# Kernel optimization log

Measured on AMD Instinct MI355X. Metric: run time of the kernel, lower is better.

The kernel has to match this reference:

```python
import jax, jax.numpy as jnp
import numpy as np

C1, C2, K, S, P, D = 128, 128, 3, 1, 1, 1
B, H, W = 16, 64, 64
K2 = K * K


def conv2d(x, w, b=None, stride=1, pad=1, dil=1):
    y = jax.lax.conv_general_dilated(
        x, w, (stride, stride), [(pad, pad), (pad, pad)],
        rhs_dilation=(dil, dil), dimension_numbers=('NCHW', 'OIHW', 'NCHW'))
    if b is not None:
        y = y + b[None, :, None, None]
    return y


def setup_inputs() -> dict:
    key = jax.random.key(0)
    ks = jax.random.split(key, 6)
    fan = C1 * K * K
    x = jax.random.normal(ks[0], (B, C1, H, W), jnp.float32)
    w_conv = jax.random.normal(ks[1], (C2, C1, K, K), jnp.float32) / np.sqrt(fan)
    # small offset / mask branch weights -> realistic small learned offsets
    w_off = jax.random.normal(ks[2], (2 * K2, C1, K, K), jnp.float32) * 0.01
    b_off = jnp.zeros((2 * K2,), jnp.float32)
    w_mask = jax.random.normal(ks[3], (K2, C1, K, K), jnp.float32) * 0.01
    b_mask = jnp.zeros((K2,), jnp.float32)
    return {'x': x, 'w_conv': w_conv, 'w_off': w_off, 'b_off': b_off,
            'w_mask': w_mask, 'b_mask': b_mask}


def _deform_conv(x, offset, mask, w_conv):
    Bv, _, Hv, Wv = x.shape
    Ho, Wo = offset.shape[2], offset.shape[3]
    off = offset.reshape(Bv, K2, 2, Ho, Wo)
    off_y, off_x = off[:, :, 0], off[:, :, 1]
    # base sampling grid: out pixel + kernel tap (stride/pad/dilation)
    hs = (jnp.arange(Ho) * S - P).astype(jnp.float32)
    ws = (jnp.arange(Wo) * S - P).astype(jnp.float32)
    n = jnp.arange(K2)
    ky = ((n // K) * D).astype(jnp.float32)
    kx = ((n % K) * D).astype(jnp.float32)
    py = off_y + hs[None, None, :, None] + ky[None, :, None, None]  # [B,K2,Ho,Wo]
    px = off_x + ws[None, None, None, :] + kx[None, :, None, None]

    y0 = jnp.floor(py)
    x0 = jnp.floor(px)
    wy1 = py - y0
    wx1 = px - x0
    wy0 = 1.0 - wy1
    wx0 = 1.0 - wx1
    y0i = y0.astype(jnp.int32)
    x0i = x0.astype(jnp.int32)

    gather = jax.vmap(lambda xb, yi, xi: xb[:, yi, xi])  # -> [B,C,K2,Ho,Wo]

    def corner(yc, xc, wgt):
        valid = (yc >= 0) & (yc < Hv) & (xc >= 0) & (xc < Wv)
        yi = jnp.clip(yc, 0, Hv - 1)
        xi = jnp.clip(xc, 0, Wv - 1)
        v = gather(x, yi, xi)
        return v * (wgt * valid)[:, None]

    samp = (corner(y0i, x0i, wy0 * wx0)
            + corner(y0i, x0i + 1, wy0 * wx1)
            + corner(y0i + 1, x0i, wy1 * wx0)
            + corner(y0i + 1, x0i + 1, wy1 * wx1))  # [B,C1,K2,Ho,Wo]
    samp = samp * mask[:, None]
    wk = w_conv.reshape(C2, C1, K2)
    return jnp.einsum('bcnhw,ocn->bohw', samp, wk)


def reference(x, w_conv, w_off, b_off, w_mask, b_mask):
    offset = conv2d(x, w_off, b_off, S, P, D)
    mask = jax.nn.sigmoid(conv2d(x, w_mask, b_mask, S, P, D))
    return _deform_conv(x, offset, mask, w_conv)
```

## Files before the change

### kernel.cpp

```cpp
#include <hip/hip_runtime.h>
#include <math.h>

#define B_   16
#define C1_  128
#define C2_  128
#define H_   64
#define W_   64
#define HW_  4096
#define NCH_ 27

typedef __attribute__((ext_vector_type(8))) short  bf16x8;
typedef __attribute__((ext_vector_type(8))) unsigned short u16x8;
typedef __attribute__((ext_vector_type(4))) float  f32x4;
typedef __attribute__((ext_vector_type(4))) unsigned int u32x4;

__device__ __forceinline__ unsigned short f2bf(float f) {
  unsigned int u = __builtin_bit_cast(unsigned int, f);
  u += 0x7fff + ((u >> 16) & 1);
  return (unsigned short)(u >> 16);
}
__device__ __forceinline__ float lo16(unsigned int u) {
  return __builtin_bit_cast(float, u << 16);
}
__device__ __forceinline__ float hi16(unsigned int u) {
  return __builtin_bit_cast(float, u & 0xffff0000u);
}

__global__ __launch_bounds__(256) void prep_k(
    const float* __restrict__ x, unsigned short* __restrict__ xcl,
    const float* __restrict__ wc, unsigned short* __restrict__ wpk,
    const float* __restrict__ w_off, const float* __restrict__ w_mask,
    unsigned short* __restrict__ wob) {
  __shared__ unsigned short tile[128][66];
  int blk = blockIdx.x;
  int t = threadIdx.x;

  if (blk < 1024) {
    int bid = blk;
    int bh = ((bid & 7) << 7) | (bid >> 3);
    int b = bh >> 6, h = bh & 63;
    int wv = t & 63, cq = t >> 6;
    const float* xb = x + ((size_t)b * 128) * HW_ + h * 64;
#pragma unroll
    for (int i = 0; i < 32; ++i) {
      int c = i * 4 + cq;
      tile[c][wv] = f2bf(xb[(size_t)c * HW_ + wv]);
    }
    __syncthreads();
    int w2 = t >> 2, cg = (t & 3) * 32;
    unsigned short* op = xcl + (((size_t)bh) * 64 + w2) * 128 + cg;
#pragma unroll
    for (int i = 0; i < 4; ++i) {
      u16x8 pk;
#pragma unroll
      for (int j = 0; j < 8; ++j) pk[j] = tile[cg + i * 8 + j][w2];
      *reinterpret_cast<u16x8*>(op + i * 8) = pk;
    }
  } else if (blk < 1024 + 576) {
    int idx = (blk - 1024) * 256 + t;
    if (idx >= 9 * 8 * 4 * 64 * 8) return;
    int j  = idx & 7;
    int l  = (idx >> 3) & 63;
    int kb = (idx >> 9) & 3;
    int ot = (idx >> 11) & 7;
    int n  = idx >> 14;
    int oc = ot * 16 + (l & 15);
    int c  = kb * 32 + (l >> 4) * 8 + j;
    wpk[idx] = f2bf(wc[(oc * 128 + c) * 9 + n]);
  } else {
    int idx = (blk - 1024 - 576) * 256 + t;
    if (idx >= 2 * 36 * 64 * 8) return;
    int j = idx & 7;
    int l = (idx >> 3) & 63;
    int rest = idx >> 9;
    int s = rest % 36;
    int nt = rest / 36;
    int ch = nt * 16 + (l & 15);
    int n = s >> 2;
    int c = (s & 3) * 32 + (l >> 4) * 8 + j;
    float v = 0.f;
    if (ch < 18) v = w_off[((ch * 128) + c) * 9 + n];
    else if (ch < 27) v = w_mask[(((ch - 18) * 128) + c) * 9 + n];
    wob[idx] = f2bf(v);
  }
}

__global__ __launch_bounds__(256) void offmask_k(
    const unsigned short* __restrict__ xcl,
    const unsigned short* __restrict__ wob,
    const float* __restrict__ b_off, const float* __restrict__ b_mask,
    float* __restrict__ om) {
  __shared__ __attribute__((aligned(16))) char xr[3 * 66 * 256];
  int bid = blockIdx.x;
  int bh = ((bid & 7) << 7) | (bid >> 3);
  int b = bh >> 6, h = bh & 63;
  int t = threadIdx.x;
  int l = t & 63, w = t >> 6;

#pragma unroll
  for (int ky = 0; ky < 3; ++ky) {
    int hh = h - 1 + ky;
    bool valid = (unsigned)hh < 64u;
    const unsigned short* src = xcl + (((size_t)b * 64 + (valid ? hh : 0)) * 64) * 128;
#pragma unroll
    for (int i = 0; i < 4; ++i) {
      int m = t + i * 256;
      int px = m >> 4;
      int c2 = (m & 15) * 16;
      unsigned off = (unsigned)((ky * 66 + px + 1) * 256 + c2) ^ (((px + 1) & 7) << 4);
      u16x8 v = {0, 0, 0, 0, 0, 0, 0, 0};
      if (valid) v = *reinterpret_cast<const u16x8*>(src + (size_t)m * 8);
      *reinterpret_cast<u16x8*>(xr + off) = v;
    }
  }
  if (t < 96) {
    int r = t >> 5, rem = t & 31;
    int slot = (rem < 16) ? 0 : 65;
    int c2 = (rem & 15) * 16;
    unsigned off = (unsigned)((r * 66 + slot) * 256 + c2) ^ ((slot & 7) << 4);
    u16x8 z = {0, 0, 0, 0, 0, 0, 0, 0};
    *reinterpret_cast<u16x8*>(xr + off) = z;
  }
  __syncthreads();

  f32x4 acc0 = (f32x4)0.f, acc1 = (f32x4)0.f;
#pragma unroll
  for (int n = 0; n < 9; ++n) {
    int ky = n / 3, kx = n % 3;
    int slot = w * 16 + (l & 15) + kx;
#pragma unroll
    for (int cs = 0; cs < 4; ++cs) {
      int s = n * 4 + cs;
      unsigned aoff = (unsigned)((ky * 66 + slot) * 256 + (l >> 4) * 16 + cs * 64)
                      ^ ((unsigned)(slot & 7) << 4);
      bf16x8 afr = *reinterpret_cast<const bf16x8*>(xr + aoff);
      bf16x8 bf0 = *reinterpret_cast<const bf16x8*>(wob + ((size_t)(0 * 36 + s) * 64 + l) * 8);
      bf16x8 bf1 = *reinterpret_cast<const bf16x8*>(wob + ((size_t)(1 * 36 + s) * 64 + l) * 8);
      acc0 = __builtin_amdgcn_mfma_f32_16x16x32_bf16(afr, bf0, acc0, 0, 0, 0);
      acc1 = __builtin_amdgcn_mfma_f32_16x16x32_bf16(afr, bf1, acc1, 0, 0, 0);
    }
  }

  int pxo = w * 16 + (l >> 4) * 4;
#pragma unroll
  for (int nt = 0; nt < 2; ++nt) {
    int ch = nt * 16 + (l & 15);
    f32x4 v = (nt == 0) ? acc0 : acc1;
    if (ch < 27) {
      float bias = (ch < 18) ? b_off[ch] : b_mask[ch - 18];
#pragma unroll
      for (int r = 0; r < 4; ++r) {
        float y = v[r] + bias;
        if (ch >= 18) y = 1.f / (1.f + __expf(-y));
        v[r] = y;
      }
      *reinterpret_cast<f32x4*>(om + ((size_t)b * NCH_ + ch) * HW_ + h * 64 + pxo) = v;
    }
  }
}

__device__ __forceinline__ bf16x8 blend4(u16x8 a, u16x8 b, u16x8 c, u16x8 d,
                                         float w0, float w1, float w2, float w3) {
  u32x4 ua = __builtin_bit_cast(u32x4, a);
  u32x4 ub = __builtin_bit_cast(u32x4, b);
  u32x4 uc = __builtin_bit_cast(u32x4, c);
  u32x4 ud = __builtin_bit_cast(u32x4, d);
  u32x4 r;
#pragma unroll
  for (int e = 0; e < 4; ++e) {
    float lo = w0 * lo16(ua[e]) + w1 * lo16(ub[e]) + w2 * lo16(uc[e]) + w3 * lo16(ud[e]);
    float hi = w0 * hi16(ua[e]) + w1 * hi16(ub[e]) + w2 * hi16(uc[e]) + w3 * hi16(ud[e]);
    unsigned ulo = __builtin_bit_cast(unsigned, lo) + 0x8000u;
    unsigned uhi = __builtin_bit_cast(unsigned, hi) + 0x8000u;
    r[e] = __builtin_amdgcn_perm(uhi, ulo, 0x07060302u);
  }
  return __builtin_bit_cast(bf16x8, r);
}

__global__ __launch_bounds__(512, 1) void dcn_k(
    const unsigned short* __restrict__ xcl,
    const unsigned short* __restrict__ wpk,
    const float* __restrict__ om,
    float* __restrict__ out) {
  __shared__ __attribute__((aligned(16))) unsigned short xrow[6 * 64 * 128];
  __shared__ __attribute__((aligned(16))) unsigned short wlds[2][16384];

  int bid = blockIdx.x;
  int bp = ((bid & 7) << 6) | (bid >> 3);
  int b = bp >> 5;
  int h0 = (bp & 31) * 2;
  int t = threadIdx.x;
  int l = t & 63;
  int w = t >> 6;
  int r = w >> 2;
  int q = w & 3;
  int h = h0 + r;

  const unsigned short* xb = xcl + ((size_t)b * HW_) * 128;
  const char* xbc = reinterpret_cast<const char*>(xb);

  int lo = max(0, h0 - 2), hi = min(63, h0 + 3);
  int nrows = hi - lo + 1;
  {
    const unsigned short* src = xb + ((size_t)lo * 64) * 128;
    int nchunks = nrows * 1024;
    for (int c = t; c < nchunks; c += 512) {
      int x = (c >> 4) & 63;
      unsigned dst = ((unsigned)c * 16) ^ (unsigned)((x & 7) << 4);
      *reinterpret_cast<u16x8*>(reinterpret_cast<char*>(xrow) + dst) =
          *reinterpret_cast<const u16x8*>(src + (size_t)c * 8);
    }
  }

  int px_l   = q * 16 + (l & 15);
  int cslice = (l >> 4) * 16;
  const float* ombr = om + (size_t)b * NCH_ * HW_ + h * 64;

  float omv[9][3];
#pragma unroll
  for (int n = 0; n < 9; ++n) {
    omv[n][0] = ombr[(2 * n) * HW_ + px_l];
    omv[n][1] = ombr[(2 * n + 1) * HW_ + px_l];
    omv[n][2] = ombr[(18 + n) * HW_ + px_l];
  }

  {
    const unsigned short* wsrc = wpk + t * 8;
    u16x8 wreg[4];
#pragma unroll
    for (int i = 0; i < 4; ++i)
      wreg[i] = *reinterpret_cast<const u16x8*>(wsrc + i * 4096);
#pragma unroll
    for (int i = 0; i < 4; ++i)
      *reinterpret_cast<u16x8*>(&wlds[0][0] + t * 8 + i * 4096) = wreg[i];
  }
  __syncthreads();

  f32x4 acc[8];
#pragma unroll
  for (int t2 = 0; t2 < 8; ++t2) acc[t2] = (f32x4)0.f;

#pragma unroll
  for (int n = 0; n < 9; ++n) {
    u16x8 wreg[4];
    if (n < 8) {
      const unsigned short* wsrc = wpk + (size_t)(n + 1) * 16384 + t * 8;
#pragma unroll
      for (int i = 0; i < 4; ++i)
        wreg[i] = *reinterpret_cast<const u16x8*>(wsrc + i * 4096);
    }

    float oy = omv[n][0];
    float ox = omv[n][1];
    float m_ = omv[n][2];
    float py  = oy + (float)(h - 1 + n / 3);
    float pxf = ox + (float)(px_l - 1 + n % 3);
    float y0f = floorf(py), x0f = floorf(pxf);
    int y0 = (int)y0f, x0 = (int)x0f;
    float wy1 = py - y0f, wx1 = pxf - x0f;
    float wy0 = 1.f - wy1, wx0 = 1.f - wx1;
    bool vy0 = (unsigned)y0 < 64u, vy1 = (unsigned)(y0 + 1) < 64u;
    bool vx0 = (unsigned)x0 < 64u, vx1 = (unsigned)(x0 + 1) < 64u;
    int y0c = min(max(y0, 0), 63), y1c = min(max(y0 + 1, 0), 63);
    int x0c = min(max(x0, 0), 63), x1c = min(max(x0 + 1, 0), 63);
    float w00 = (vy0 && vx0) ? wy0 * wx0 * m_ : 0.f;
    float w01 = (vy0 && vx1) ? wy0 * wx1 * m_ : 0.f;
    float w10 = (vy1 && vx0) ? wy1 * wx0 * m_ : 0.f;
    float w11 = (vy1 && vx1) ? wy1 * wx1 * m_ : 0.f;

    const unsigned short* wb = &wlds[n & 1][0];
    bool inlds = ((unsigned)(y0c - lo) < (unsigned)nrows) &&
                 ((unsigned)(y1c - lo) < (unsigned)nrows);

    if (__all(inlds)) {
      int p00 = (y0c - lo) * 64 + x0c, p01 = (y0c - lo) * 64 + x1c;
      int p10 = (y1c - lo) * 64 + x0c, p11 = (y1c - lo) * 64 + x1c;
      unsigned s00 = (unsigned)((x0c & 7) << 4), s01 = (unsigned)((x1c & 7) << 4);
      const char* xr = reinterpret_cast<const char*>(xrow);
#pragma unroll
      for (int kb = 0; kb < 4; ++kb) {
        int cb = kb * 64 + cslice;
        u16x8 c0 = *reinterpret_cast<const u16x8*>(xr + (((unsigned)(p00 * 256 + cb)) ^ s00));
        u16x8 c1 = *reinterpret_cast<const u16x8*>(xr + (((unsigned)(p01 * 256 + cb)) ^ s01));
        u16x8 c2 = *reinterpret_cast<const u16x8*>(xr + (((unsigned)(p10 * 256 + cb)) ^ s00));
        u16x8 c3 = *reinterpret_cast<const u16x8*>(xr + (((unsigned)(p11 * 256 + cb)) ^ s01));
        bf16x8 afr = blend4(c0, c1, c2, c3, w00, w01, w10, w11);
#pragma unroll
        for (int t2 = 0; t2 < 8; ++t2) {
          bf16x8 bfr = *reinterpret_cast<const bf16x8*>(
              wb + ((t2 * 4 + kb) * 64 + l) * 8);
          acc[t2] = __builtin_amdgcn_mfma_f32_16x16x32_bf16(afr, bfr, acc[t2], 0, 0, 0);
        }
      }
    } else {
      int i00 = (y0c * 64 + x0c) * 256, i01 = (y0c * 64 + x1c) * 256;
      int i10 = (y1c * 64 + x0c) * 256, i11 = (y1c * 64 + x1c) * 256;
#pragma unroll
      for (int kb = 0; kb < 4; ++kb) {
        int cb = kb * 64 + cslice;
        u16x8 c0 = *reinterpret_cast<const u16x8*>(xbc + i00 + cb);
        u16x8 c1 = *reinterpret_cast<const u16x8*>(xbc + i01 + cb);
        u16x8 c2 = *reinterpret_cast<const u16x8*>(xbc + i10 + cb);
        u16x8 c3 = *reinterpret_cast<const u16x8*>(xbc + i11 + cb);
        bf16x8 afr = blend4(c0, c1, c2, c3, w00, w01, w10, w11);
#pragma unroll
        for (int t2 = 0; t2 < 8; ++t2) {
          bf16x8 bfr = *reinterpret_cast<const bf16x8*>(
              wb + ((t2 * 4 + kb) * 64 + l) * 8);
          acc[t2] = __builtin_amdgcn_mfma_f32_16x16x32_bf16(afr, bfr, acc[t2], 0, 0, 0);
        }
      }
    }

    if (n < 8) {
      unsigned short* wdst = &wlds[(n + 1) & 1][0];
#pragma unroll
      for (int i = 0; i < 4; ++i)
        *reinterpret_cast<u16x8*>(wdst + t * 8 + i * 4096) = wreg[i];
      __syncthreads();
    }
  }

  int oc_l = l & 15;
  int px0 = q * 16 + (l >> 4) * 4;
#pragma unroll
  for (int t2 = 0; t2 < 8; ++t2) {
    int oc = t2 * 16 + oc_l;
    *reinterpret_cast<f32x4*>(out + ((size_t)b * C2_ + oc) * HW_ + h * 64 + px0) = acc[t2];
  }
}

extern "C" void kernel_launch(void* const* d_in, const int* in_sizes, int n_in,
                              void* d_out, int out_size, void* d_ws, size_t ws_size,
                              hipStream_t stream) {
  const float* x      = (const float*)d_in[0];
  const float* w_conv = (const float*)d_in[1];
  const float* w_off  = (const float*)d_in[2];
  const float* b_off  = (const float*)d_in[3];
  const float* w_mask = (const float*)d_in[4];
  const float* b_mask = (const float*)d_in[5];
  float* out = (float*)d_out;

  float* om = (float*)d_ws;
  unsigned short* wpk = (unsigned short*)(om + (size_t)B_ * NCH_ * HW_);
  unsigned short* wob = wpk + 147456;
  unsigned short* xcl = wob + 36864;

  hipLaunchKernelGGL(prep_k, dim3(1024 + 576 + 144), dim3(256), 0, stream,
                     x, xcl, w_conv, wpk, w_off, w_mask, wob);
  hipLaunchKernelGGL(offmask_k, dim3(B_ * H_), dim3(256), 0, stream,
                     xcl, wob, b_off, b_mask, om);
  hipLaunchKernelGGL(dcn_k, dim3(512), dim3(512), 0, stream,
                     xcl, wpk, om, out);
}
```

Baseline: 84.02 us.

## Fuse offset/mask convolution into deformable conv kernel via shared memory

Removes the separate offmask_k launch and computes the offset and mask 3x3 convolution inside dcn_k. It reuses the input rows already staged in LDS and stages the 27 per-pixel results in the second weight buffer in LDS. This drops one kernel launch and the global write and read of the offset/mask tensor. In exchange, each dcn block does extra MFMA work and adds barriers before its main loop, which runs at only one block per CU.

After: 89.16 us. +6.1%, slower.

```diff
diff --git a/kernel.cpp b/kernel.cpp
--- a/kernel.cpp
+++ b/kernel.cpp
@@ -85,80 +85,6 @@
   }
 }
 
-__global__ __launch_bounds__(256) void offmask_k(
-    const unsigned short* __restrict__ xcl,
-    const unsigned short* __restrict__ wob,
-    const float* __restrict__ b_off, const float* __restrict__ b_mask,
-    float* __restrict__ om) {
-  __shared__ __attribute__((aligned(16))) char xr[3 * 66 * 256];
-  int bid = blockIdx.x;
-  int bh = ((bid & 7) << 7) | (bid >> 3);
-  int b = bh >> 6, h = bh & 63;
-  int t = threadIdx.x;
-  int l = t & 63, w = t >> 6;
-
-#pragma unroll
-  for (int ky = 0; ky < 3; ++ky) {
-    int hh = h - 1 + ky;
-    bool valid = (unsigned)hh < 64u;
-    const unsigned short* src = xcl + (((size_t)b * 64 + (valid ? hh : 0)) * 64) * 128;
-#pragma unroll
-    for (int i = 0; i < 4; ++i) {
-      int m = t + i * 256;
-      int px = m >> 4;
-      int c2 = (m & 15) * 16;
-      unsigned off = (unsigned)((ky * 66 + px + 1) * 256 + c2) ^ (((px + 1) & 7) << 4);
-      u16x8 v = {0, 0, 0, 0, 0, 0, 0, 0};
-      if (valid) v = *reinterpret_cast<const u16x8*>(src + (size_t)m * 8);
-      *reinterpret_cast<u16x8*>(xr + off) = v;
-    }
-  }
-  if (t < 96) {
-    int r = t >> 5, rem = t & 31;
-    int slot = (rem < 16) ? 0 : 65;
-    int c2 = (rem & 15) * 16;
-    unsigned off = (unsigned)((r * 66 + slot) * 256 + c2) ^ ((slot & 7) << 4);
-    u16x8 z = {0, 0, 0, 0, 0, 0, 0, 0};
-    *reinterpret_cast<u16x8*>(xr + off) = z;
-  }
-  __syncthreads();
-
-  f32x4 acc0 = (f32x4)0.f, acc1 = (f32x4)0.f;
-#pragma unroll
-  for (int n = 0; n < 9; ++n) {
-    int ky = n / 3, kx = n % 3;
-    int slot = w * 16 + (l & 15) + kx;
-#pragma unroll
-    for (int cs = 0; cs < 4; ++cs) {
-      int s = n * 4 + cs;
-      unsigned aoff = (unsigned)((ky * 66 + slot) * 256 + (l >> 4) * 16 + cs * 64)
-                      ^ ((unsigned)(slot & 7) << 4);
-      bf16x8 afr = *reinterpret_cast<const bf16x8*>(xr + aoff);
-      bf16x8 bf0 = *reinterpret_cast<const bf16x8*>(wob + ((size_t)(0 * 36 + s) * 64 + l) * 8);
-      bf16x8 bf1 = *reinterpret_cast<const bf16x8*>(wob + ((size_t)(1 * 36 + s) * 64 + l) * 8);
-      acc0 = __builtin_amdgcn_mfma_f32_16x16x32_bf16(afr, bf0, acc0, 0, 0, 0);
-      acc1 = __builtin_amdgcn_mfma_f32_16x16x32_bf16(afr, bf1, acc1, 0, 0, 0);
-    }
-  }
-
-  int pxo = w * 16 + (l >> 4) * 4;
-#pragma unroll
-  for (int nt = 0; nt < 2; ++nt) {
-    int ch = nt * 16 + (l & 15);
-    f32x4 v = (nt == 0) ? acc0 : acc1;
-    if (ch < 27) {
-      float bias = (ch < 18) ? b_off[ch] : b_mask[ch - 18];
-#pragma unroll
-      for (int r = 0; r < 4; ++r) {
-        float y = v[r] + bias;
-        if (ch >= 18) y = 1.f / (1.f + __expf(-y));
-        v[r] = y;
-      }
-      *reinterpret_cast<f32x4*>(om + ((size_t)b * NCH_ + ch) * HW_ + h * 64 + pxo) = v;
-    }
-  }
-}
-
 __device__ __forceinline__ bf16x8 blend4(u16x8 a, u16x8 b, u16x8 c, u16x8 d,
                                          float w0, float w1, float w2, float w3) {
   u32x4 ua = __builtin_bit_cast(u32x4, a);
@@ -180,7 +106,8 @@
 __global__ __launch_bounds__(512, 1) void dcn_k(
     const unsigned short* __restrict__ xcl,
     const unsigned short* __restrict__ wpk,
-    const float* __restrict__ om,
+    const unsigned short* __restrict__ wob,
+    const float* __restrict__ b_off, const float* __restrict__ b_mask,
     float* __restrict__ out) {
   __shared__ __attribute__((aligned(16))) unsigned short xrow[6 * 64 * 128];
   __shared__ __attribute__((aligned(16))) unsigned short wlds[2][16384];
@@ -212,18 +139,6 @@
     }
   }
 
-  int px_l   = q * 16 + (l & 15);
-  int cslice = (l >> 4) * 16;
-  const float* ombr = om + (size_t)b * NCH_ * HW_ + h * 64;
-
-  float omv[9][3];
-#pragma unroll
-  for (int n = 0; n < 9; ++n) {
-    omv[n][0] = ombr[(2 * n) * HW_ + px_l];
-    omv[n][1] = ombr[(2 * n + 1) * HW_ + px_l];
-    omv[n][2] = ombr[(18 + n) * HW_ + px_l];
-  }
-
   {
     const unsigned short* wsrc = wpk + t * 8;
     u16x8 wreg[4];
@@ -233,6 +148,62 @@
 #pragma unroll
     for (int i = 0; i < 4; ++i)
       *reinterpret_cast<u16x8*>(&wlds[0][0] + t * 8 + i * 4096) = wreg[i];
+  }
+  __syncthreads();
+
+  int px_l   = q * 16 + (l & 15);
+  int cslice = (l >> 4) * 16;
+  const char* xr = reinterpret_cast<const char*>(xrow);
+
+  f32x4 oacc0 = (f32x4)0.f, oacc1 = (f32x4)0.f;
+#pragma unroll
+  for (int n = 0; n < 9; ++n) {
+    int ky = n / 3, kx = n % 3;
+    int row_a = h - 1 + ky;
+    int col = px_l + kx - 1;
+    bool valid = ((unsigned)row_a < 64u) && ((unsigned)col < 64u);
+    int p = (row_a - lo) * 64 + col;
+    unsigned sxz = (unsigned)((col & 7) << 4);
+#pragma unroll
+    for (int cs = 0; cs < 4; ++cs) {
+      int s = n * 4 + cs;
+      bf16x8 afr = {0, 0, 0, 0, 0, 0, 0, 0};
+      if (valid)
+        afr = *reinterpret_cast<const bf16x8*>(
+            xr + (((unsigned)(p * 256 + cs * 64 + cslice)) ^ sxz));
+      bf16x8 bf0 = *reinterpret_cast<const bf16x8*>(wob + ((size_t)(0 * 36 + s) * 64 + l) * 8);
+      bf16x8 bf1 = *reinterpret_cast<const bf16x8*>(wob + ((size_t)(1 * 36 + s) * 64 + l) * 8);
+      oacc0 = __builtin_amdgcn_mfma_f32_16x16x32_bf16(afr, bf0, oacc0, 0, 0, 0);
+      oacc1 = __builtin_amdgcn_mfma_f32_16x16x32_bf16(afr, bf1, oacc1, 0, 0, 0);
+    }
+  }
+  float* omld = reinterpret_cast<float*>(&wlds[1][0]);
+#pragma unroll
+  for (int nt = 0; nt < 2; ++nt) {
+    int ch = nt * 16 + (l & 15);
+    f32x4 v = (nt == 0) ? oacc0 : oacc1;
+    if (ch < 27) {
+      float bias = (ch < 18) ? b_off[ch] : b_mask[ch - 18];
+#pragma unroll
+      for (int r4 = 0; r4 < 4; ++r4) {
+        float y = v[r4] + bias;
+        if (ch >= 18) y = 1.f / (1.f + __expf(-y));
+        int pxo = q * 16 + (l >> 4) * 4 + r4;
+        omld[(r * 64 + pxo) * 28 + ch] = y;
+      }
+    }
+  }
+  __syncthreads();
+
+  float omv[9][3];
+  {
+    const float* base = &omld[(r * 64 + px_l) * 28];
+#pragma unroll
+    for (int n = 0; n < 9; ++n) {
+      omv[n][0] = base[2 * n];
+      omv[n][1] = base[2 * n + 1];
+      omv[n][2] = base[18 + n];
+    }
   }
   __syncthreads();
 
@@ -276,7 +247,6 @@
       int p00 = (y0c - lo) * 64 + x0c, p01 = (y0c - lo) * 64 + x1c;
       int p10 = (y1c - lo) * 64 + x0c, p11 = (y1c - lo) * 64 + x1c;
       unsigned s00 = (unsigned)((x0c & 7) << 4), s01 = (unsigned)((x1c & 7) << 4);
-      const char* xr = reinterpret_cast<const char*>(xrow);
 #pragma unroll
       for (int kb = 0; kb < 4; ++kb) {
         int cb = kb * 64 + cslice;
@@ -348,8 +318,6 @@
 
   hipLaunchKernelGGL(prep_k, dim3(1024 + 576 + 144), dim3(256), 0, stream,
                      x, xcl, w_conv, wpk, w_off, w_mask, wob);
-  hipLaunchKernelGGL(offmask_k, dim3(B_ * H_), dim3(256), 0, stream,
-                     xcl, wob, b_off, b_mask, om);
   hipLaunchKernelGGL(dcn_k, dim3(512), dim3(512), 0, stream,
-                     xcl, wpk, om, out);
-}
+                     xcl, wpk, wob, b_off, b_mask, out);
+}
```
